# Kernel optimization log

Hardware: AMD Instinct MI355X
Metric: run time of the kernel (lower is better)

## Reference

```python
import jax, jax.numpy as jnp
import numpy as np

K = 256           # number of selected features (init kwarg k)
NUM_SAMPLES = 8   # init kwarg num_samples
BATCH = 256
NUM_FEATURES = 20000


def setup_inputs() -> dict:
    key = jax.random.key(0)
    logits = jax.random.normal(key, (BATCH, NUM_FEATURES, 1), dtype=jnp.float32)
    return {"logits": logits, "tau": 1, "training": 0}


def reference(logits, tau, training):
    # Eval branch of SubsetLayer.forward (training=False).
    # logits: [B, N, 1]
    B, N, _ = logits.shape
    scores = logits[..., 0]                       # [B, N]
    _, idx = jax.lax.top_k(scores, K)             # idx: [B, K]
    # k-hot mask built directly by scatter (equivalent to one_hot(...).sum(1))
    khot = jnp.zeros((B, N), dtype=jnp.float32)
    khot = khot.at[jnp.arange(B)[:, None], idx].set(1.0)  # [B, N]
    # unsqueeze(0).unsqueeze(-1).expand(num_samples, -1, -1, -1)
    out = jnp.broadcast_to(khot[None, :, :, None], (NUM_SAMPLES, B, N, 1))
    return out
```

## Files before the change

kernel.cpp:

```cpp
#include <hip/hip_runtime.h>

#define BATCH   256
#define NFEAT   20000
#define NVEC    (NFEAT / 4)
#define KSEL    256
#define NSAMP   8

typedef unsigned long long u64;
typedef float __attribute__((ext_vector_type(4))) f32x4;

__device__ __forceinline__ unsigned fmap(float f) {
    unsigned u = __float_as_uint(f);
    return (u & 0x80000000u) ? ~u : (u | 0x80000000u);
}

__device__ __forceinline__ void pick64(const unsigned* arr, int w, int lane,
                                       int* s_idx, int* s_w) {
    unsigned c = arr[63 - lane];
    unsigned p = c;
#pragma unroll
    for (int off = 1; off < 64; off <<= 1) {
        unsigned t = __shfl_up(p, off);
        if (lane >= off) p += t;
    }
    unsigned long long m = __ballot(p >= (unsigned)w);
    if (m) {
        int l = __ffsll(m) - 1;
        if (lane == l) { *s_idx = 63 - l; *s_w = w - (int)(p - c); }
    } else if (lane == 0) { *s_idx = 0; *s_w = 1; }
}

__global__ __launch_bounds__(1024) void topk_select(const float* __restrict__ logits,
                                                    u64* __restrict__ rowthr) {
    const int b = blockIdx.x, tid = threadIdx.x;
    const int lane = tid & 63, wave = tid >> 6;
    const float4* __restrict__ row4 = (const float4*)(logits + (size_t)b * NFEAT);

    __shared__ unsigned hist[4096];
    __shared__ unsigned csum[64];
    __shared__ int s_d, s_w;
    __shared__ u64 s_thr;
    __shared__ int s_run, s_cut, s_wc[16];

    float4 v[5];
#pragma unroll
    for (int j = 0; j < 5; ++j) {
        const int i4 = tid + j * 1024;
        v[j] = row4[(i4 < NVEC) ? i4 : (NVEC - 1)];
    }
#pragma unroll
    for (int j = 0; j < 4; ++j) hist[tid + j * 1024] = 0;
    __syncthreads();

    unsigned kk[5][4];
#pragma unroll
    for (int j = 0; j < 5; ++j) {
        kk[j][0] = fmap(v[j].x); kk[j][1] = fmap(v[j].y);
        kk[j][2] = fmap(v[j].z); kk[j][3] = fmap(v[j].w);
    }
#pragma unroll
    for (int j = 0; j < 4; ++j) {
#pragma unroll
        for (int e = 0; e < 4; ++e) atomicAdd(&hist[kk[j][e] >> 20], 1u);
    }
    if (tid + 4096 < NVEC) {
#pragma unroll
        for (int e = 0; e < 4; ++e) atomicAdd(&hist[kk[4][e] >> 20], 1u);
    }
    __syncthreads();

    unsigned P; int w;
    {
#pragma unroll
        for (int j = 0; j < 4; ++j) {
            const int cc = wave * 4 + j;
            unsigned x = hist[cc * 64 + lane];
#pragma unroll
            for (int off = 32; off; off >>= 1) x += __shfl_down(x, off);
            if (lane == 0) csum[cc] = x;
        }
        __syncthreads();
        if (wave == 0) pick64(csum, KSEL, lane, &s_d, &s_w);
        __syncthreads();
        const int chunk = s_d; const int w0 = s_w;
        if (wave == 0) pick64(&hist[chunk * 64], w0, lane, &s_d, &s_w);
        __syncthreads();
        P = (unsigned)(chunk * 64 + s_d);
        w = s_w;
    }
    unsigned cnt = hist[P];
    int shift = 20;

    while (cnt > 1u && shift > 0) {
        const int nb  = (shift >= 8) ? 8 : shift;
        const int nsh = shift - nb;
        const int NB  = 1 << nb;
        const int nz  = (NB > 64) ? NB : 64;
        __syncthreads();
        if (tid < nz) hist[tid] = 0;
        if (tid >= 4 && tid < 64) csum[tid] = 0;
        __syncthreads();

#pragma unroll
        for (int j = 0; j < 5; ++j) {
            const int i4 = tid + j * 1024;
            if (i4 < NVEC) {
#pragma unroll
                for (int e = 0; e < 4; ++e) {
                    const unsigned k = kk[j][e];
                    if ((k >> shift) == P)
                        atomicAdd(&hist[(k >> nsh) & (unsigned)(NB - 1)], 1u);
                }
            }
        }
        __syncthreads();

        unsigned d;
        if (NB > 64) {
            if (wave < 4) {
                unsigned x = hist[wave * 64 + lane];
#pragma unroll
                for (int off = 32; off; off >>= 1) x += __shfl_down(x, off);
                if (lane == 0) csum[wave] = x;
            }
            __syncthreads();
            if (wave == 0) pick64(csum, w, lane, &s_d, &s_w);
            __syncthreads();
            const int chunk2 = s_d; const int w1 = s_w;
            if (wave == 0) pick64(&hist[chunk2 * 64], w1, lane, &s_d, &s_w);
            __syncthreads();
            d = (unsigned)(chunk2 * 64 + s_d);
        } else {
            if (wave == 0) pick64(hist, w, lane, &s_d, &s_w);
            __syncthreads();
            d = (unsigned)s_d;
        }
        w = s_w;
        cnt = hist[d];
        P = (P << nb) | d;
        shift = nsh;
    }

    if (cnt == 1u) {
#pragma unroll
        for (int j = 0; j < 5; ++j) {
            const int i4 = tid + j * 1024;
            if (i4 < NVEC) {
#pragma unroll
                for (int e = 0; e < 4; ++e) {
                    const unsigned k = kk[j][e];
                    if ((k >> shift) == P)
                        s_thr = ((u64)k << 32) | (unsigned)~(4 * i4 + e);
                }
            }
        }
        __syncthreads();
    } else {
        if (tid == 0) { s_run = 0; s_cut = 0; }
        __syncthreads();
#pragma unroll 1
        for (int j = 0; j < 5; ++j) {
            const int i4 = tid + j * 1024;
            bool eq[4];
            int cnt4 = 0;
#pragma unroll
            for (int e = 0; e < 4; ++e) {
                eq[e] = (i4 < NVEC) && (kk[j][e] == P);
                cnt4 += eq[e] ? 1 : 0;
            }
            unsigned p = (unsigned)cnt4;
#pragma unroll
            for (int off = 1; off < 64; off <<= 1) {
                unsigned t = __shfl_up(p, off);
                if (lane >= off) p += t;
            }
            const unsigned excl = p - (unsigned)cnt4;
            if (lane == 63) s_wc[wave] = (int)p;
            __syncthreads();
            int off0 = s_run + (int)excl;
            for (int x = 0; x < wave; ++x) off0 += s_wc[x];
#pragma unroll
            for (int e = 0; e < 4; ++e) {
                if (eq[e]) { if (off0 == w - 1) s_cut = 4 * i4 + e; ++off0; }
            }
            __syncthreads();
            if (tid == 0) { int t = 0; for (int x = 0; x < 16; ++x) t += s_wc[x]; s_run += t; }
            __syncthreads();
            if (s_run >= w) break;
        }
        if (tid == 0) s_thr = ((u64)P << 32) | (unsigned)~s_cut;
        __syncthreads();
    }

    if (tid == 0) rowthr[b] = s_thr;
}

__global__ __launch_bounds__(256) void write_out(const float* __restrict__ logits,
                                                 const u64* __restrict__ rowthr,
                                                 float* __restrict__ out) {
    const int b = blockIdx.y;
    const int q = blockIdx.x * 256 + threadIdx.x;
    if (q >= NVEC) return;

    const u64 thr = rowthr[b];
    const unsigned thr_k = (unsigned)(thr >> 32);
    const unsigned thr_l = (unsigned)thr;
    const int n = q * 4;
    const float4 v = *reinterpret_cast<const float4*>(logits + (size_t)b * NFEAT + n);

    f32x4 m;
    {
        const float* vf = &v.x;
#pragma unroll
        for (int j = 0; j < 4; ++j) {
            const unsigned k = fmap(vf[j]);
            const bool sel = (k > thr_k) || (k == thr_k && (unsigned)~(n + j) >= thr_l);
            m[j] = sel ? 1.0f : 0.0f;
        }
    }

#pragma unroll
    for (int s = 0; s < NSAMP; ++s) {
        *reinterpret_cast<f32x4*>(out + ((size_t)s * BATCH + b) * NFEAT + n) = m;
    }
}

extern "C" void kernel_launch(void* const* d_in, const int* in_sizes, int n_in,
                              void* d_out, int out_size, void* d_ws, size_t ws_size,
                              hipStream_t stream) {
    const float* logits = (const float*)d_in[0];
    float* out = (float*)d_out;
    u64* rowthr = (u64*)d_ws;

    topk_select<<<BATCH, 1024, 0, stream>>>(logits, rowthr);

    dim3 grid((NVEC + 255) / 256, BATCH);
    write_out<<<grid, 256, 0, stream>>>(logits, rowthr, out);
}
```

Before: 41.81 us.

## Warp-specialize single kernel: half block selects top-k while other half zero-fills output

Merges the two kernels into one launch per row. Within each block, 512 threads run the radix top-k selection using custom workgroup-scope atomic barriers, while the other 512 threads write zeros to all 8 sample copies of the row at the same time. When selection finishes, the selected indices go into an LDS list and the writer threads scatter 1.0 into those positions. This drops the second launch and the re-read of logits, and overlaps the output stores with the selection work. In exchange, selection runs on half as many threads with more registers each, the barriers spin-wait, and the final ones are scattered scalar stores that must land after the zero stores.

```diff
diff --git a/kernel.cpp b/kernel.cpp
--- a/kernel.cpp
+++ b/kernel.cpp
@@ -5,6 +5,8 @@
 #define NVEC    (NFEAT / 4)
 #define KSEL    256
 #define NSAMP   8
+#define SELT    512
+#define NBATCH  10
 
 typedef unsigned long long u64;
 typedef float __attribute__((ext_vector_type(4))) f32x4;
@@ -30,198 +32,235 @@
     } else if (lane == 0) { *s_idx = 0; *s_w = 1; }
 }
 
-__global__ __launch_bounds__(1024) void topk_select(const float* __restrict__ logits,
-                                                    u64* __restrict__ rowthr) {
+__device__ __forceinline__ void group_bar(int* ctr, int lane, int* phase, int nw) {
+    *phase += nw;
+    if (lane == 0)
+        __hip_atomic_fetch_add(ctr, 1, __ATOMIC_ACQ_REL, __HIP_MEMORY_SCOPE_WORKGROUP);
+    while (__hip_atomic_load(ctr, __ATOMIC_ACQUIRE, __HIP_MEMORY_SCOPE_WORKGROUP) < *phase)
+        __builtin_amdgcn_s_sleep(1);
+}
+
+__global__ __launch_bounds__(1024) void topk_ws(const float* __restrict__ logits,
+                                                float* __restrict__ out) {
     const int b = blockIdx.x, tid = threadIdx.x;
-    const int lane = tid & 63, wave = tid >> 6;
-    const float4* __restrict__ row4 = (const float4*)(logits + (size_t)b * NFEAT);
+    const int lane = tid & 63;
+    const size_t BN = (size_t)BATCH * NFEAT;
+    float* const outb = out + (size_t)b * NFEAT;
 
     __shared__ unsigned hist[4096];
     __shared__ unsigned csum[64];
+    __shared__ unsigned idxlist[SELT];
     __shared__ int s_d, s_w;
     __shared__ u64 s_thr;
-    __shared__ int s_run, s_cut, s_wc[16];
-
-    float4 v[5];
-#pragma unroll
-    for (int j = 0; j < 5; ++j) {
-        const int i4 = tid + j * 1024;
-        v[j] = row4[(i4 < NVEC) ? i4 : (NVEC - 1)];
-    }
-#pragma unroll
-    for (int j = 0; j < 4; ++j) hist[tid + j * 1024] = 0;
+    __shared__ unsigned s_nidx;
+    __shared__ int s_selbar, s_wrbar, s_flag;
+    __shared__ int s_run, s_cut, s_wc[8];
+
+    if (tid == 0) { s_selbar = 0; s_wrbar = 0; s_flag = 0; s_nidx = 0; }
     __syncthreads();
 
-    unsigned kk[5][4];
-#pragma unroll
-    for (int j = 0; j < 5; ++j) {
-        kk[j][0] = fmap(v[j].x); kk[j][1] = fmap(v[j].y);
-        kk[j][2] = fmap(v[j].z); kk[j][3] = fmap(v[j].w);
-    }
-#pragma unroll
-    for (int j = 0; j < 4; ++j) {
-#pragma unroll
-        for (int e = 0; e < 4; ++e) atomicAdd(&hist[kk[j][e] >> 20], 1u);
-    }
-    if (tid + 4096 < NVEC) {
-#pragma unroll
-        for (int e = 0; e < 4; ++e) atomicAdd(&hist[kk[4][e] >> 20], 1u);
-    }
-    __syncthreads();
-
-    unsigned P; int w;
-    {
-#pragma unroll
-        for (int j = 0; j < 4; ++j) {
-            const int cc = wave * 4 + j;
-            unsigned x = hist[cc * 64 + lane];
-#pragma unroll
-            for (int off = 32; off; off >>= 1) x += __shfl_down(x, off);
-            if (lane == 0) csum[cc] = x;
-        }
-        __syncthreads();
-        if (wave == 0) pick64(csum, KSEL, lane, &s_d, &s_w);
-        __syncthreads();
-        const int chunk = s_d; const int w0 = s_w;
-        if (wave == 0) pick64(&hist[chunk * 64], w0, lane, &s_d, &s_w);
-        __syncthreads();
-        P = (unsigned)(chunk * 64 + s_d);
-        w = s_w;
-    }
-    unsigned cnt = hist[P];
-    int shift = 20;
-
-    while (cnt > 1u && shift > 0) {
-        const int nb  = (shift >= 8) ? 8 : shift;
-        const int nsh = shift - nb;
-        const int NB  = 1 << nb;
-        const int nz  = (NB > 64) ? NB : 64;
-        __syncthreads();
-        if (tid < nz) hist[tid] = 0;
-        if (tid >= 4 && tid < 64) csum[tid] = 0;
-        __syncthreads();
-
-#pragma unroll
-        for (int j = 0; j < 5; ++j) {
-            const int i4 = tid + j * 1024;
+    if (tid < SELT) {
+        const int t = tid;
+        const int wave = t >> 6;
+        int ph = 0;
+        const float4* __restrict__ row4 = (const float4*)(logits + (size_t)b * NFEAT);
+
+        float4 v[NBATCH];
+#pragma unroll
+        for (int j = 0; j < NBATCH; ++j) {
+            const int i4 = t + j * SELT;
+            v[j] = row4[(i4 < NVEC) ? i4 : (NVEC - 1)];
+        }
+#pragma unroll
+        for (int j = 0; j < 8; ++j) hist[t + j * SELT] = 0;
+
+        unsigned kk[NBATCH][4];
+#pragma unroll
+        for (int j = 0; j < NBATCH; ++j) {
+            kk[j][0] = fmap(v[j].x); kk[j][1] = fmap(v[j].y);
+            kk[j][2] = fmap(v[j].z); kk[j][3] = fmap(v[j].w);
+        }
+        group_bar(&s_selbar, lane, &ph, 8);
+
+#pragma unroll
+        for (int j = 0; j < NBATCH; ++j) {
+            const int i4 = t + j * SELT;
+            if (i4 < NVEC) {
+#pragma unroll
+                for (int e = 0; e < 4; ++e) atomicAdd(&hist[kk[j][e] >> 20], 1u);
+            }
+        }
+        group_bar(&s_selbar, lane, &ph, 8);
+
+        unsigned P; int w;
+        {
+#pragma unroll
+            for (int jj = 0; jj < 8; ++jj) {
+                const int cc = wave * 8 + jj;
+                unsigned x = hist[cc * 64 + lane];
+#pragma unroll
+                for (int off = 32; off; off >>= 1) x += __shfl_down(x, off);
+                if (lane == 0) csum[cc] = x;
+            }
+            group_bar(&s_selbar, lane, &ph, 8);
+            if (wave == 0) pick64(csum, KSEL, lane, &s_d, &s_w);
+            group_bar(&s_selbar, lane, &ph, 8);
+            const int chunk = s_d; const int w0 = s_w;
+            if (wave == 0) pick64(&hist[chunk * 64], w0, lane, &s_d, &s_w);
+            group_bar(&s_selbar, lane, &ph, 8);
+            P = (unsigned)(chunk * 64 + s_d);
+            w = s_w;
+        }
+        unsigned cnt = hist[P];
+        int shift = 20;
+
+        while (cnt > 1u && shift > 0) {
+            const int nb  = (shift >= 8) ? 8 : shift;
+            const int nsh = shift - nb;
+            const int NB  = 1 << nb;
+            const int nz  = (NB > 64) ? NB : 64;
+            group_bar(&s_selbar, lane, &ph, 8);
+            for (int i = t; i < nz; i += SELT) hist[i] = 0;
+            if (t >= 4 && t < 64) csum[t] = 0;
+            group_bar(&s_selbar, lane, &ph, 8);
+
+#pragma unroll
+            for (int j = 0; j < NBATCH; ++j) {
+                const int i4 = t + j * SELT;
+                if (i4 < NVEC) {
+#pragma unroll
+                    for (int e = 0; e < 4; ++e) {
+                        const unsigned k = kk[j][e];
+                        if ((k >> shift) == P)
+                            atomicAdd(&hist[(k >> nsh) & (unsigned)(NB - 1)], 1u);
+                    }
+                }
+            }
+            group_bar(&s_selbar, lane, &ph, 8);
+
+            unsigned d;
+            if (NB > 64) {
+                if (wave < 4) {
+                    unsigned x = hist[wave * 64 + lane];
+#pragma unroll
+                    for (int off = 32; off; off >>= 1) x += __shfl_down(x, off);
+                    if (lane == 0) csum[wave] = x;
+                }
+                group_bar(&s_selbar, lane, &ph, 8);
+                if (wave == 0) pick64(csum, w, lane, &s_d, &s_w);
+                group_bar(&s_selbar, lane, &ph, 8);
+                const int c2 = s_d; const int w1 = s_w;
+                if (wave == 0) pick64(&hist[c2 * 64], w1, lane, &s_d, &s_w);
+                group_bar(&s_selbar, lane, &ph, 8);
+                d = (unsigned)(c2 * 64 + s_d);
+            } else {
+                if (wave == 0) pick64(hist, w, lane, &s_d, &s_w);
+                group_bar(&s_selbar, lane, &ph, 8);
+                d = (unsigned)s_d;
+            }
+            w = s_w;
+            cnt = hist[d];
+            P = (P << nb) | d;
+            shift = nsh;
+        }
+
+        if (cnt == 1u) {
+#pragma unroll
+            for (int j = 0; j < NBATCH; ++j) {
+                const int i4 = t + j * SELT;
+                if (i4 < NVEC) {
+#pragma unroll
+                    for (int e = 0; e < 4; ++e) {
+                        const unsigned k = kk[j][e];
+                        if ((k >> shift) == P)
+                            s_thr = ((u64)k << 32) | (unsigned)~(4 * i4 + e);
+                    }
+                }
+            }
+            group_bar(&s_selbar, lane, &ph, 8);
+        } else {
+            if (t == 0) { s_run = 0; s_cut = 0; }
+            group_bar(&s_selbar, lane, &ph, 8);
+#pragma unroll 1
+            for (int j = 0; j < NBATCH; ++j) {
+                const int i4 = t + j * SELT;
+                bool eq[4];
+                int cnt4 = 0;
+#pragma unroll
+                for (int e = 0; e < 4; ++e) {
+                    eq[e] = (i4 < NVEC) && (kk[j][e] == P);
+                    cnt4 += eq[e] ? 1 : 0;
+                }
+                unsigned p = (unsigned)cnt4;
+#pragma unroll
+                for (int off = 1; off < 64; off <<= 1) {
+                    unsigned tt = __shfl_up(p, off);
+                    if (lane >= off) p += tt;
+                }
+                const unsigned excl = p - (unsigned)cnt4;
+                if (lane == 63) s_wc[wave] = (int)p;
+                group_bar(&s_selbar, lane, &ph, 8);
+                int off0 = s_run + (int)excl;
+                for (int x = 0; x < wave; ++x) off0 += s_wc[x];
+#pragma unroll
+                for (int e = 0; e < 4; ++e) {
+                    if (eq[e]) { if (off0 == w - 1) s_cut = 4 * i4 + e; ++off0; }
+                }
+                group_bar(&s_selbar, lane, &ph, 8);
+                if (t == 0) { int s = 0; for (int x = 0; x < 8; ++x) s += s_wc[x]; s_run += s; }
+                group_bar(&s_selbar, lane, &ph, 8);
+                if (s_run >= w) break;
+            }
+            if (t == 0) s_thr = ((u64)P << 32) | (unsigned)~s_cut;
+            group_bar(&s_selbar, lane, &ph, 8);
+        }
+
+        const u64 thr = s_thr;
+        const unsigned thr_k = (unsigned)(thr >> 32);
+        const unsigned thr_l = (unsigned)thr;
+#pragma unroll
+        for (int j = 0; j < NBATCH; ++j) {
+            const int i4 = t + j * SELT;
             if (i4 < NVEC) {
 #pragma unroll
                 for (int e = 0; e < 4; ++e) {
                     const unsigned k = kk[j][e];
-                    if ((k >> shift) == P)
-                        atomicAdd(&hist[(k >> nsh) & (unsigned)(NB - 1)], 1u);
-                }
-            }
-        }
-        __syncthreads();
-
-        unsigned d;
-        if (NB > 64) {
-            if (wave < 4) {
-                unsigned x = hist[wave * 64 + lane];
-#pragma unroll
-                for (int off = 32; off; off >>= 1) x += __shfl_down(x, off);
-                if (lane == 0) csum[wave] = x;
-            }
-            __syncthreads();
-            if (wave == 0) pick64(csum, w, lane, &s_d, &s_w);
-            __syncthreads();
-            const int chunk2 = s_d; const int w1 = s_w;
-            if (wave == 0) pick64(&hist[chunk2 * 64], w1, lane, &s_d, &s_w);
-            __syncthreads();
-            d = (unsigned)(chunk2 * 64 + s_d);
-        } else {
-            if (wave == 0) pick64(hist, w, lane, &s_d, &s_w);
-            __syncthreads();
-            d = (unsigned)s_d;
-        }
-        w = s_w;
-        cnt = hist[d];
-        P = (P << nb) | d;
-        shift = nsh;
-    }
-
-    if (cnt == 1u) {
-#pragma unroll
-        for (int j = 0; j < 5; ++j) {
-            const int i4 = tid + j * 1024;
-            if (i4 < NVEC) {
-#pragma unroll
-                for (int e = 0; e < 4; ++e) {
-                    const unsigned k = kk[j][e];
-                    if ((k >> shift) == P)
-                        s_thr = ((u64)k << 32) | (unsigned)~(4 * i4 + e);
-                }
-            }
-        }
-        __syncthreads();
+                    const int n = 4 * i4 + e;
+                    const bool sel = (k > thr_k) || (k == thr_k && (unsigned)~n >= thr_l);
+                    if (sel) {
+                        unsigned pos = atomicAdd(&s_nidx, 1u);
+                        idxlist[pos & (SELT - 1)] = (unsigned)n;
+                    }
+                }
+            }
+        }
+        group_bar(&s_selbar, lane, &ph, 8);
+        if (t == 0)
+            __hip_atomic_store(&s_flag, 1, __ATOMIC_RELEASE, __HIP_MEMORY_SCOPE_WORKGROUP);
     } else {
-        if (tid == 0) { s_run = 0; s_cut = 0; }
-        __syncthreads();
-#pragma unroll 1
-        for (int j = 0; j < 5; ++j) {
-            const int i4 = tid + j * 1024;
-            bool eq[4];
-            int cnt4 = 0;
-#pragma unroll
-            for (int e = 0; e < 4; ++e) {
-                eq[e] = (i4 < NVEC) && (kk[j][e] == P);
-                cnt4 += eq[e] ? 1 : 0;
-            }
-            unsigned p = (unsigned)cnt4;
-#pragma unroll
-            for (int off = 1; off < 64; off <<= 1) {
-                unsigned t = __shfl_up(p, off);
-                if (lane >= off) p += t;
-            }
-            const unsigned excl = p - (unsigned)cnt4;
-            if (lane == 63) s_wc[wave] = (int)p;
-            __syncthreads();
-            int off0 = s_run + (int)excl;
-            for (int x = 0; x < wave; ++x) off0 += s_wc[x];
-#pragma unroll
-            for (int e = 0; e < 4; ++e) {
-                if (eq[e]) { if (off0 == w - 1) s_cut = 4 * i4 + e; ++off0; }
-            }
-            __syncthreads();
-            if (tid == 0) { int t = 0; for (int x = 0; x < 16; ++x) t += s_wc[x]; s_run += t; }
-            __syncthreads();
-            if (s_run >= w) break;
-        }
-        if (tid == 0) s_thr = ((u64)P << 32) | (unsigned)~s_cut;
-        __syncthreads();
-    }
-
-    if (tid == 0) rowthr[b] = s_thr;
-}
-
-__global__ __launch_bounds__(256) void write_out(const float* __restrict__ logits,
-                                                 const u64* __restrict__ rowthr,
-                                                 float* __restrict__ out) {
-    const int b = blockIdx.y;
-    const int q = blockIdx.x * 256 + threadIdx.x;
-    if (q >= NVEC) return;
-
-    const u64 thr = rowthr[b];
-    const unsigned thr_k = (unsigned)(thr >> 32);
-    const unsigned thr_l = (unsigned)thr;
-    const int n = q * 4;
-    const float4 v = *reinterpret_cast<const float4*>(logits + (size_t)b * NFEAT + n);
-
-    f32x4 m;
-    {
-        const float* vf = &v.x;
-#pragma unroll
-        for (int j = 0; j < 4; ++j) {
-            const unsigned k = fmap(vf[j]);
-            const bool sel = (k > thr_k) || (k == thr_k && (unsigned)~(n + j) >= thr_l);
-            m[j] = sel ? 1.0f : 0.0f;
-        }
-    }
-
-#pragma unroll
-    for (int s = 0; s < NSAMP; ++s) {
-        *reinterpret_cast<f32x4*>(out + ((size_t)s * BATCH + b) * NFEAT + n) = m;
+        const int t2 = tid - SELT;
+        int ph = 0;
+        const f32x4 z4 = {0.0f, 0.0f, 0.0f, 0.0f};
+
+#pragma unroll
+        for (int s = 0; s < NSAMP; ++s) {
+            float* const base = outb + (size_t)s * BN;
+            for (int i = t2; i < NVEC; i += SELT)
+                *reinterpret_cast<f32x4*>(base + 4 * i) = z4;
+        }
+        asm volatile("s_waitcnt vmcnt(0)" ::: "memory");
+        group_bar(&s_wrbar, lane, &ph, 8);
+
+        while (__hip_atomic_load(&s_flag, __ATOMIC_ACQUIRE, __HIP_MEMORY_SCOPE_WORKGROUP) == 0)
+            __builtin_amdgcn_s_sleep(2);
+
+        const unsigned nsel = s_nidx;
+        if (t2 < nsel) {
+            const unsigned idx = idxlist[t2];
+#pragma unroll
+            for (int s = 0; s < NSAMP; ++s)
+                outb[(size_t)s * BN + idx] = 1.0f;
+        }
     }
 }
 
@@ -230,10 +269,7 @@
                               hipStream_t stream) {
     const float* logits = (const float*)d_in[0];
     float* out = (float*)d_out;
-    u64* rowthr = (u64*)d_ws;
-
-    topk_select<<<BATCH, 1024, 0, stream>>>(logits, rowthr);
-
-    dim3 grid((NVEC + 255) / 256, BATCH);
-    write_out<<<grid, 256, 0, stream>>>(logits, rowthr, out);
-}
+    (void)d_ws; (void)ws_size;
+
+    topk_ws<<<BATCH, 1024, 0, stream>>>(logits, out);
+}
```

New measurement: 35.90 us. 14.1% less time.
